# Optimization experiments

Hardware: AMD Instinct MI355X
Metric: run time of the kernel (lower is better)

## Reference

```python
import math
import jax, jax.numpy as jnp
import numpy as np

B, S, D, H = 2, 2048, 768, 12
DK = D // H  # 64
SCALE = math.sqrt(DK)


def setup_inputs() -> dict:
    key = jax.random.key(0)
    ks = jax.random.split(key, 8)
    q = jax.random.normal(ks[0], (B, S, D), dtype=jnp.float32)
    k = jax.random.normal(ks[1], (B, S, D), dtype=jnp.float32)
    v = jax.random.normal(ks[2], (B, S, D), dtype=jnp.float32)
    # causal mask (1 = attend, 0 = masked), per docstring [B, S, S]
    mask = jnp.broadcast_to(jnp.tril(jnp.ones((S, S), dtype=jnp.int32)), (B, S, S))
    std = 1.0 / math.sqrt(D)
    Wq = jax.random.uniform(ks[3], (D, D), jnp.float32, -std, std)
    Wk = jax.random.uniform(ks[4], (D, D), jnp.float32, -std, std)
    Wv = jax.random.uniform(ks[5], (D, D), jnp.float32, -std, std)
    Wo = jax.random.uniform(ks[6], (D, D), jnp.float32, -std, std)
    bo = jax.random.uniform(ks[7], (D,), jnp.float32, -std, std)
    return {"query": q, "key": k, "value": v, "mask": mask,
            "Wq": Wq, "Wk": Wk, "Wv": Wv, "Wo": Wo, "bo": bo}


def reference(query, key, value, mask, Wq, Wk, Wv, Wo, bo):
    # torch Linear: y = x @ W.T (no bias for q/k/v)
    Q = (query @ Wq.T).reshape(B, S, H, DK)  # [B,S,H,dk]
    K = (key @ Wk.T).reshape(B, S, H, DK)
    V = (value @ Wv.T).reshape(B, S, H, DK)
    # scores [B,H,S,S]
    scores = jnp.einsum('bqhd,bkhd->bhqk', Q, K) / SCALE
    scores = jnp.where(mask[:, None, :, :] == 0, jnp.float32(-1e9), scores)
    attention_weights = jax.nn.softmax(scores, axis=-1)
    # dropout is identity in eval mode (reference is deterministic)
    out = jnp.einsum('bhqk,bkhd->bqhd', attention_weights, V).reshape(B, S, D)
    output = out @ Wo.T + bo
    return output, attention_weights
```

## Files before the change

### kernel.cpp

```cpp
#include <hip/hip_runtime.h>
#include <cmath>

constexpr int B = 2, S = 2048, D = 768, H = 12, DK = 64;
constexpr int QKV_N = B * H * S * DK;
constexpr float INV_SCALE = 0.125f;


using bf16x8 = __attribute__((ext_vector_type(8))) short;
using bf16x4 = __attribute__((ext_vector_type(4))) short;
using f32x4  = __attribute__((ext_vector_type(4))) float;

#define DEVI __device__ __forceinline__

DEVI unsigned short f2hi(float x) { union { float f; unsigned u; } c; c.f = x; return (unsigned short)(c.u >> 16); }
DEVI float hi2f(unsigned short h) { union { unsigned u; float f; } c; c.u = (unsigned)h << 16; return c.f; }

DEVI void split8(const float* a, bf16x8& h8, bf16x8& l8) {
  #pragma unroll
  for (int i = 0; i < 8; i++) {
    unsigned short h = f2hi(a[i]);
    h8[i] = (short)h;
    l8[i] = (short)f2hi(a[i] - hi2f(h));
  }
}

DEVI f32x4 mfma3_32(bf16x8 ah, bf16x8 al, bf16x8 bh, bf16x8 bl, f32x4 acc) {
  acc = __builtin_amdgcn_mfma_f32_16x16x32_bf16(al, bh, acc, 0, 0, 0);
  acc = __builtin_amdgcn_mfma_f32_16x16x32_bf16(ah, bl, acc, 0, 0, 0);
  acc = __builtin_amdgcn_mfma_f32_16x16x32_bf16(ah, bh, acc, 0, 0, 0);
  return acc;
}

#if __has_builtin(__builtin_amdgcn_mfma_f32_16x16x16bf16_1k)
DEVI f32x4 mfma16(bf16x4 a, bf16x4 b, f32x4 c) { return __builtin_amdgcn_mfma_f32_16x16x16bf16_1k(a, b, c, 0, 0, 0); }
#elif __has_builtin(__builtin_amdgcn_mfma_f32_16x16x16_bf16_1k)
DEVI f32x4 mfma16(bf16x4 a, bf16x4 b, f32x4 c) { return __builtin_amdgcn_mfma_f32_16x16x16_bf16_1k(a, b, c, 0, 0, 0); }
#elif __has_builtin(__builtin_amdgcn_mfma_f32_16x16x16_bf16)
DEVI f32x4 mfma16(bf16x4 a, bf16x4 b, f32x4 c) { return __builtin_amdgcn_mfma_f32_16x16x16_bf16(a, b, c, 0, 0, 0); }
#else
DEVI f32x4 mfma16(bf16x4 a, bf16x4 b, f32x4 c) {
  asm volatile("v_mfma_f32_16x16x16_bf16 %0, %1, %2, %0" : "+v"(c) : "v"(a), "v"(b));
  return c;
}
#endif

constexpr int PAD = 40;

__global__ __launch_bounds__(512)
void k_qkv_mfma(const float* __restrict__ Xq, const float* __restrict__ Xk,
                const float* __restrict__ Xv,
                const float* __restrict__ Wq, const float* __restrict__ Wk,
                const float* __restrict__ Wv,
                short* __restrict__ Qh, short* __restrict__ Ql,
                short* __restrict__ Kh, short* __restrict__ Kl,
                short* __restrict__ Vh, short* __restrict__ Vl) {
  __shared__ __align__(16) short Ah[128][PAD], Al[128][PAD];
  __shared__ __align__(16) short Bh[128][PAD], Bl[128][PAD];
  const int z = blockIdx.z;
  const float* __restrict__ X = (z == 0) ? Xq : (z == 1) ? Xk : Xv;
  const float* __restrict__ W = (z == 0) ? Wq : (z == 1) ? Wk : Wv;
  short* __restrict__ O_h = (z == 0) ? Qh : (z == 1) ? Kh : Vh;
  short* __restrict__ O_l = (z == 0) ? Ql : (z == 1) ? Kl : Vl;
  const float sc = (z == 0) ? INV_SCALE : 1.0f;
  const int m0 = blockIdx.y * 128, n0 = blockIdx.x * 128;
  const int t = threadIdx.x, wave = t >> 6, lane = t & 63;
  const int wm = (wave >> 1) * 32, wn = (wave & 1) * 64;
  const int srow = t >> 2, sch = (t & 3) * 8;
  const int fr = lane & 15, fk = (lane >> 4) * 8;

  f32x4 acc[2][4];
  #pragma unroll
  for (int i = 0; i < 2; i++)
    #pragma unroll
    for (int j = 0; j < 4; j++) acc[i][j] = (f32x4){0.f, 0.f, 0.f, 0.f};

  for (int k0 = 0; k0 < D; k0 += 32) {
    float abuf[8], bbuf[8];
    *(float4*)&abuf[0] = *(const float4*)&X[(size_t)(m0 + srow) * D + k0 + sch];
    *(float4*)&abuf[4] = *(const float4*)&X[(size_t)(m0 + srow) * D + k0 + sch + 4];
    *(float4*)&bbuf[0] = *(const float4*)&W[(size_t)(n0 + srow) * D + k0 + sch];
    *(float4*)&bbuf[4] = *(const float4*)&W[(size_t)(n0 + srow) * D + k0 + sch + 4];
    bf16x8 h8, l8;
    split8(abuf, h8, l8);
    *(bf16x8*)&Ah[srow][sch] = h8; *(bf16x8*)&Al[srow][sch] = l8;
    split8(bbuf, h8, l8);
    *(bf16x8*)&Bh[srow][sch] = h8; *(bf16x8*)&Bl[srow][sch] = l8;
    __syncthreads();
    bf16x8 a_h[2], a_l[2];
    #pragma unroll
    for (int st = 0; st < 2; st++) {
      a_h[st] = *(const bf16x8*)&Ah[wm + st * 16 + fr][fk];
      a_l[st] = *(const bf16x8*)&Al[wm + st * 16 + fr][fk];
    }
    #pragma unroll
    for (int ct = 0; ct < 4; ct++) {
      bf16x8 b_h = *(const bf16x8*)&Bh[wn + ct * 16 + fr][fk];
      bf16x8 b_l = *(const bf16x8*)&Bl[wn + ct * 16 + fr][fk];
      acc[0][ct] = mfma3_32(a_h[0], a_l[0], b_h, b_l, acc[0][ct]);
      acc[1][ct] = mfma3_32(a_h[1], a_l[1], b_h, b_l, acc[1][ct]);
    }
    __syncthreads();
  }
  #pragma unroll
  for (int st = 0; st < 2; st++)
    #pragma unroll
    for (int ct = 0; ct < 4; ct++)
      #pragma unroll
      for (int r = 0; r < 4; r++) {
        int m = m0 + wm + st * 16 + (lane >> 4) * 4 + r;
        int n = n0 + wn + ct * 16 + (lane & 15);
        int bb = m >> 11, ss = m & (S - 1), hx = n >> 6, dd = n & 63;
        size_t idx = (((size_t)bb * H + hx) * S + ss) * DK + dd;
        float x = acc[st][ct][r] * sc;
        unsigned short xh = f2hi(x);
        O_h[idx] = (short)xh;
        O_l[idx] = (short)f2hi(x - hi2f(xh));
      }
}

constexpr int PADK = 80;
constexpr int PADV = 136;
constexpr int PADC = 132;
constexpr int K_BYTES = 128 * PADK * 2;
constexpr int V_BYTES = 64 * PADV * 2;
constexpr int SMEM_BYTES = 2 * K_BYTES + 2 * V_BYTES;

__global__ __launch_bounds__(512)
void k_attn_fused(const short* __restrict__ Qsh, const short* __restrict__ Qsl,
                  const short* __restrict__ Ksg, const short* __restrict__ Klg,
                  const short* __restrict__ Vsg, const short* __restrict__ Vlg,
                  float* __restrict__ attn, float* __restrict__ ctx) {
  __shared__ __align__(16) char smem[SMEM_BYTES];
  short* Ksh = (short*)smem;
  short* Ksl = (short*)(smem + K_BYTES);
  short* VTh = (short*)(smem + 2 * K_BYTES);
  short* VTl = (short*)(smem + 2 * K_BYTES + V_BYTES);
  float* ctxT = (float*)smem;

  const int qt = 15 - (int)blockIdx.x;
  const int bh = blockIdx.y;
  const int q0 = qt * 128;
  const int kend = (qt + 1) * 128;
  const int t = threadIdx.x, wave = t >> 6, lane = t & 63;
  const int g = lane >> 4, c = lane & 15;
  const int wq = wave * 16;
  const int q = q0 + wq + c;
  const size_t hrow = (size_t)bh * S;

  {
    const int ncols = S - kend;
    if (ncols > 0) {
      const float4 z4 = {0.f, 0.f, 0.f, 0.f};
      for (int rr = 0; rr < 128; ++rr) {
        float* rowp = &attn[(hrow + q0 + rr) * S + kend];
        for (int cc = t * 4; cc < ncols; cc += 2048)
          *(float4*)&rowp[cc] = z4;
      }
    }
  }

  bf16x8 qh0, ql0, qh1, ql1;
  {
    const size_t qb = (hrow + q) * DK + g * 8;
    qh0 = *(const bf16x8*)&Qsh[qb];
    ql0 = *(const bf16x8*)&Qsl[qb];
    qh1 = *(const bf16x8*)&Qsh[qb + 32];
    ql1 = *(const bf16x8*)&Qsl[qb + 32];
  }

  const int srow = t >> 2, sch = (t & 3) * 16;

  float m_run = -3.0e38f, l_run = 0.f;
  for (int kt = 0; kt <= qt; ++kt) {
    {
      const size_t gk = (hrow + (size_t)(kt * 128 + srow)) * DK + sch;
      *(bf16x8*)&Ksh[srow * PADK + sch]     = *(const bf16x8*)&Ksg[gk];
      *(bf16x8*)&Ksh[srow * PADK + sch + 8] = *(const bf16x8*)&Ksg[gk + 8];
      *(bf16x8*)&Ksl[srow * PADK + sch]     = *(const bf16x8*)&Klg[gk];
      *(bf16x8*)&Ksl[srow * PADK + sch + 8] = *(const bf16x8*)&Klg[gk + 8];
    }
    __syncthreads();
    #pragma unroll
    for (int f = 0; f < 8; ++f) {
      const int krow = f * 16 + c;
      bf16x8 kh0 = *(const bf16x8*)&Ksh[krow * PADK + g * 8];
      bf16x8 kl0 = *(const bf16x8*)&Ksl[krow * PADK + g * 8];
      bf16x8 kh1 = *(const bf16x8*)&Ksh[krow * PADK + 32 + g * 8];
      bf16x8 kl1 = *(const bf16x8*)&Ksl[krow * PADK + 32 + g * 8];
      f32x4 s = {0.f, 0.f, 0.f, 0.f};
      s = mfma3_32(kh0, kl0, qh0, ql0, s);
      s = mfma3_32(kh1, kl1, qh1, ql1, s);
      const int kb = kt * 128 + f * 16 + g * 4;
      float tm = -3.0e38f;
      #pragma unroll
      for (int r = 0; r < 4; ++r) {
        float sv = (kb + r <= q) ? s[r] : -3.0e38f;
        tm = fmaxf(tm, sv);
      }
      if (tm > m_run) { l_run *= __expf(m_run - tm); m_run = tm; }
      #pragma unroll
      for (int r = 0; r < 4; ++r)
        l_run += (kb + r <= q) ? __expf(s[r] - m_run) : 0.f;
    }
    __syncthreads();
  }
  #pragma unroll
  for (int off = 16; off <= 32; off <<= 1) {
    float mo = __shfl_xor(m_run, off);
    float lo2 = __shfl_xor(l_run, off);
    float mn = fmaxf(m_run, mo);
    l_run = l_run * __expf(m_run - mn) + lo2 * __expf(mo - mn);
    m_run = mn;
  }
  const float inv_l = 1.0f / l_run;

  f32x4 cacc[4];
  #pragma unroll
  for (int dt = 0; dt < 4; ++dt) cacc[dt] = (f32x4){0.f, 0.f, 0.f, 0.f};

  for (int kt = 0; kt <= qt; ++kt) {
    {
      const size_t gk = (hrow + (size_t)(kt * 128 + srow)) * DK + sch;
      *(bf16x8*)&Ksh[srow * PADK + sch]     = *(const bf16x8*)&Ksg[gk];
      *(bf16x8*)&Ksh[srow * PADK + sch + 8] = *(const bf16x8*)&Ksg[gk + 8];
      *(bf16x8*)&Ksl[srow * PADK + sch]     = *(const bf16x8*)&Klg[gk];
      *(bf16x8*)&Ksl[srow * PADK + sch + 8] = *(const bf16x8*)&Klg[gk + 8];
      bf16x8 vh0 = *(const bf16x8*)&Vsg[gk];
      bf16x8 vh1 = *(const bf16x8*)&Vsg[gk + 8];
      bf16x8 vl0 = *(const bf16x8*)&Vlg[gk];
      bf16x8 vl1 = *(const bf16x8*)&Vlg[gk + 8];
      #pragma unroll
      for (int i = 0; i < 8; ++i) {
        VTh[(sch + i) * PADV + srow]     = vh0[i];
        VTh[(sch + 8 + i) * PADV + srow] = vh1[i];
        VTl[(sch + i) * PADV + srow]     = vl0[i];
        VTl[(sch + 8 + i) * PADV + srow] = vl1[i];
      }
    }
    __syncthreads();
    #pragma unroll
    for (int f = 0; f < 8; ++f) {
      const int krow = f * 16 + c;
      bf16x8 kh0 = *(const bf16x8*)&Ksh[krow * PADK + g * 8];
      bf16x8 kl0 = *(const bf16x8*)&Ksl[krow * PADK + g * 8];
      bf16x8 kh1 = *(const bf16x8*)&Ksh[krow * PADK + 32 + g * 8];
      bf16x8 kl1 = *(const bf16x8*)&Ksl[krow * PADK + 32 + g * 8];
      f32x4 s = {0.f, 0.f, 0.f, 0.f};
      s = mfma3_32(kh0, kl0, qh0, ql0, s);
      s = mfma3_32(kh1, kl1, qh1, ql1, s);
      const int kb = kt * 128 + f * 16 + g * 4;
      float p[4];
      #pragma unroll
      for (int r = 0; r < 4; ++r) {
        float e = __expf(s[r] - m_run) * inv_l;
        p[r] = (kb + r <= q) ? e : 0.f;
      }
      float4 pw = {p[0], p[1], p[2], p[3]};
      *(float4*)&attn[(hrow + q) * S + kb] = pw;
      bf16x4 ph, pl;
      #pragma unroll
      for (int r = 0; r < 4; ++r) {
        unsigned short xh = f2hi(p[r]);
        ph[r] = (short)xh;
        pl[r] = (short)f2hi(p[r] - hi2f(xh));
      }
      #pragma unroll
      for (int dt = 0; dt < 4; ++dt) {
        const int vr = dt * 16 + c;
        bf16x4 vh4 = *(const bf16x4*)&VTh[vr * PADV + f * 16 + g * 4];
        bf16x4 vl4 = *(const bf16x4*)&VTl[vr * PADV + f * 16 + g * 4];
        cacc[dt] = mfma16(vl4, ph, cacc[dt]);
        cacc[dt] = mfma16(vh4, pl, cacc[dt]);
        cacc[dt] = mfma16(vh4, ph, cacc[dt]);
      }
    }
    __syncthreads();
  }

  #pragma unroll
  for (int dt = 0; dt < 4; ++dt)
    #pragma unroll
    for (int r = 0; r < 4; ++r)
      ctxT[(dt * 16 + g * 4 + r) * PADC + wq + c] = cacc[dt][r];
  __syncthreads();
  {
    const int row = t >> 2, ch2 = (t & 3) * 16;
    float buf[16];
    #pragma unroll
    for (int i = 0; i < 16; ++i) buf[i] = ctxT[(ch2 + i) * PADC + row];
    float* cp = &ctx[(hrow + q0 + row) * DK + ch2];
    #pragma unroll
    for (int j = 0; j < 4; ++j)
      *(float4*)&cp[j * 4] = *(const float4*)&buf[j * 4];
  }
}

__global__ __launch_bounds__(512)
void k_oproj_mfma(const float* __restrict__ ctx, const float* __restrict__ Wo,
                  const float* __restrict__ bo, float* __restrict__ out) {
  __shared__ __align__(16) short Ah[128][PAD], Al[128][PAD];
  __shared__ __align__(16) short Bh[128][PAD], Bl[128][PAD];
  const int m0 = blockIdx.y * 128, n0 = blockIdx.x * 128;
  const int t = threadIdx.x, wave = t >> 6, lane = t & 63;
  const int wm = (wave >> 1) * 32, wn = (wave & 1) * 64;
  const int srow = t >> 2, sch = (t & 3) * 8;
  const int fr = lane & 15, fk = (lane >> 4) * 8;

  f32x4 acc[2][4];
  #pragma unroll
  for (int i = 0; i < 2; i++)
    #pragma unroll
    for (int j = 0; j < 4; j++) acc[i][j] = (f32x4){0.f, 0.f, 0.f, 0.f};

  const int am = m0 + srow;
  const int abb = am >> 11, ass = am & (S - 1);
  for (int k0 = 0; k0 < D; k0 += 32) {
    float abuf[8], bbuf[8];
    int kk2 = k0 + sch, hx = kk2 >> 6, dd = kk2 & 63;
    const float* pa = &ctx[(((size_t)abb * H + hx) * S + ass) * DK + dd];
    *(float4*)&abuf[0] = *(const float4*)&pa[0];
    *(float4*)&abuf[4] = *(const float4*)&pa[4];
    *(float4*)&bbuf[0] = *(const float4*)&Wo[(size_t)(n0 + srow) * D + k0 + sch];
    *(float4*)&bbuf[4] = *(const float4*)&Wo[(size_t)(n0 + srow) * D + k0 + sch + 4];
    bf16x8 h8, l8;
    split8(abuf, h8, l8);
    *(bf16x8*)&Ah[srow][sch] = h8; *(bf16x8*)&Al[srow][sch] = l8;
    split8(bbuf, h8, l8);
    *(bf16x8*)&Bh[srow][sch] = h8; *(bf16x8*)&Bl[srow][sch] = l8;
    __syncthreads();
    bf16x8 a_h[2], a_l[2];
    #pragma unroll
    for (int st = 0; st < 2; st++) {
      a_h[st] = *(const bf16x8*)&Ah[wm + st * 16 + fr][fk];
      a_l[st] = *(const bf16x8*)&Al[wm + st * 16 + fr][fk];
    }
    #pragma unroll
    for (int ct = 0; ct < 4; ct++) {
      bf16x8 b_h = *(const bf16x8*)&Bh[wn + ct * 16 + fr][fk];
      bf16x8 b_l = *(const bf16x8*)&Bl[wn + ct * 16 + fr][fk];
      acc[0][ct] = mfma3_32(a_h[0], a_l[0], b_h, b_l, acc[0][ct]);
      acc[1][ct] = mfma3_32(a_h[1], a_l[1], b_h, b_l, acc[1][ct]);
    }
    __syncthreads();
  }
  #pragma unroll
  for (int st = 0; st < 2; st++)
    #pragma unroll
    for (int ct = 0; ct < 4; ct++)
      #pragma unroll
      for (int r = 0; r < 4; r++) {
        int m = m0 + wm + st * 16 + (lane >> 4) * 4 + r;
        int n = n0 + wn + ct * 16 + (lane & 15);
        out[(size_t)m * D + n] = acc[st][ct][r] + bo[n];
      }
}

extern "C" void kernel_launch(void* const* d_in, const int* in_sizes, int n_in,
                              void* d_out, int out_size, void* d_ws, size_t ws_size,
                              hipStream_t stream) {
  (void)in_sizes; (void)n_in; (void)out_size; (void)ws_size;
  const float* q  = (const float*)d_in[0];
  const float* k  = (const float*)d_in[1];
  const float* v  = (const float*)d_in[2];
  const float* Wq = (const float*)d_in[4];
  const float* Wk = (const float*)d_in[5];
  const float* Wv = (const float*)d_in[6];
  const float* Wo = (const float*)d_in[7];
  const float* bo = (const float*)d_in[8];

  float* out  = (float*)d_out;
  float* attn = out + (size_t)B * S * D;

  short* Qh = (short*)d_ws;
  short* Ql = Qh + (size_t)QKV_N;
  short* Kh = Ql + (size_t)QKV_N;
  short* Kl = Kh + (size_t)QKV_N;
  short* Vh = Kl + (size_t)QKV_N;
  short* Vl = Vh + (size_t)QKV_N;
  float* ctx = (float*)(Vl + (size_t)QKV_N);

  k_qkv_mfma<<<dim3(6, 32, 3), 512, 0, stream>>>(q, k, v, Wq, Wk, Wv,
                                                 Qh, Ql, Kh, Kl, Vh, Vl);
  k_attn_fused<<<dim3(16, 24), 512, 0, stream>>>(Qh, Ql, Kh, Kl, Vh, Vl, attn, ctx);
  k_oproj_mfma<<<dim3(6, 32), 512, 0, stream>>>(ctx, Wo, bo, out);
}
```

Before: 743.2 us.

## Shrink attention tiles to 64 rows, prefetch K/V into registers, swizzle V transpose

The fused attention kernel now uses 64-query tiles with 256-thread blocks (32x24 grid), which doubles block count and should improve occupancy and causal load balance. K/V tiles for the next iteration are loaded into registers during compute on the current tile, hiding global latency behind the MFMA work. The transposed V store/read uses an XOR swizzle with smaller padding to cut LDS bank conflicts and shared memory footprint. Smaller tiles add more barriers per key and reload K/V more often across blocks, and register prefetch raises register pressure.

```diff
diff --git a/kernel.cpp b/kernel.cpp
--- a/kernel.cpp
+++ b/kernel.cpp
@@ -118,42 +118,41 @@
       }
 }
 
-constexpr int PADK = 80;
-constexpr int PADV = 136;
-constexpr int PADC = 132;
-constexpr int K_BYTES = 128 * PADK * 2;
-constexpr int V_BYTES = 64 * PADV * 2;
-constexpr int SMEM_BYTES = 2 * K_BYTES + 2 * V_BYTES;
-
-__global__ __launch_bounds__(512)
+constexpr int PADK2 = 68;
+constexpr int PADV2 = 68;
+constexpr int PADC2 = 65;
+constexpr int KB2   = 64 * PADK2;
+constexpr int VB2   = 64 * PADV2;
+constexpr int SMEM2 = (2 * KB2 + 2 * VB2) * 2;
+
+__global__ __launch_bounds__(256, 4)
 void k_attn_fused(const short* __restrict__ Qsh, const short* __restrict__ Qsl,
                   const short* __restrict__ Ksg, const short* __restrict__ Klg,
                   const short* __restrict__ Vsg, const short* __restrict__ Vlg,
                   float* __restrict__ attn, float* __restrict__ ctx) {
-  __shared__ __align__(16) char smem[SMEM_BYTES];
+  __shared__ __align__(16) char smem[SMEM2];
   short* Ksh = (short*)smem;
-  short* Ksl = (short*)(smem + K_BYTES);
-  short* VTh = (short*)(smem + 2 * K_BYTES);
-  short* VTl = (short*)(smem + 2 * K_BYTES + V_BYTES);
+  short* Ksl = Ksh + KB2;
+  short* VTh = Ksl + KB2;
+  short* VTl = VTh + VB2;
   float* ctxT = (float*)smem;
 
-  const int qt = 15 - (int)blockIdx.x;
+  const int jt = 31 - (int)blockIdx.x;
   const int bh = blockIdx.y;
-  const int q0 = qt * 128;
-  const int kend = (qt + 1) * 128;
+  const int q0 = jt * 64;
   const int t = threadIdx.x, wave = t >> 6, lane = t & 63;
   const int g = lane >> 4, c = lane & 15;
-  const int wq = wave * 16;
-  const int q = q0 + wq + c;
+  const int q = q0 + wave * 16 + c;
   const size_t hrow = (size_t)bh * S;
 
   {
-    const int ncols = S - kend;
+    const int zc0 = q0 + 64;
+    const int ncols = S - zc0;
     if (ncols > 0) {
       const float4 z4 = {0.f, 0.f, 0.f, 0.f};
-      for (int rr = 0; rr < 128; ++rr) {
-        float* rowp = &attn[(hrow + q0 + rr) * S + kend];
-        for (int cc = t * 4; cc < ncols; cc += 2048)
+      for (int rr = 0; rr < 64; ++rr) {
+        float* rowp = &attn[(hrow + q0 + rr) * S + zc0];
+        for (int cc = t * 4; cc < ncols; cc += 1024)
           *(float4*)&rowp[cc] = z4;
       }
     }
@@ -162,47 +161,57 @@
   bf16x8 qh0, ql0, qh1, ql1;
   {
     const size_t qb = (hrow + q) * DK + g * 8;
-    qh0 = *(const bf16x8*)&Qsh[qb];
-    ql0 = *(const bf16x8*)&Qsl[qb];
-    qh1 = *(const bf16x8*)&Qsh[qb + 32];
-    ql1 = *(const bf16x8*)&Qsl[qb + 32];
-  }
-
-  const int srow = t >> 2, sch = (t & 3) * 16;
+    qh0 = *(const bf16x8*)&Qsh[qb];      ql0 = *(const bf16x8*)&Qsl[qb];
+    qh1 = *(const bf16x8*)&Qsh[qb + 32]; ql1 = *(const bf16x8*)&Qsl[qb + 32];
+  }
+
+  const int srow = t >> 2;
+  const int sch = (t & 3) * 16;
+  const int vcol = srow ^ ((t & 3) * 8);
 
   float m_run = -3.0e38f, l_run = 0.f;
-  for (int kt = 0; kt <= qt; ++kt) {
+  {
+    bf16x8 kr[4];
     {
-      const size_t gk = (hrow + (size_t)(kt * 128 + srow)) * DK + sch;
-      *(bf16x8*)&Ksh[srow * PADK + sch]     = *(const bf16x8*)&Ksg[gk];
-      *(bf16x8*)&Ksh[srow * PADK + sch + 8] = *(const bf16x8*)&Ksg[gk + 8];
-      *(bf16x8*)&Ksl[srow * PADK + sch]     = *(const bf16x8*)&Klg[gk];
-      *(bf16x8*)&Ksl[srow * PADK + sch + 8] = *(const bf16x8*)&Klg[gk + 8];
-    }
-    __syncthreads();
-    #pragma unroll
-    for (int f = 0; f < 8; ++f) {
-      const int krow = f * 16 + c;
-      bf16x8 kh0 = *(const bf16x8*)&Ksh[krow * PADK + g * 8];
-      bf16x8 kl0 = *(const bf16x8*)&Ksl[krow * PADK + g * 8];
-      bf16x8 kh1 = *(const bf16x8*)&Ksh[krow * PADK + 32 + g * 8];
-      bf16x8 kl1 = *(const bf16x8*)&Ksl[krow * PADK + 32 + g * 8];
-      f32x4 s = {0.f, 0.f, 0.f, 0.f};
-      s = mfma3_32(kh0, kl0, qh0, ql0, s);
-      s = mfma3_32(kh1, kl1, qh1, ql1, s);
-      const int kb = kt * 128 + f * 16 + g * 4;
-      float tm = -3.0e38f;
+      const size_t gk = (hrow + (size_t)srow) * DK + sch;
+      kr[0] = *(const bf16x8*)&Ksg[gk]; kr[1] = *(const bf16x8*)&Ksg[gk + 8];
+      kr[2] = *(const bf16x8*)&Klg[gk]; kr[3] = *(const bf16x8*)&Klg[gk + 8];
+    }
+    for (int kt = 0; kt <= jt; ++kt) {
+      __syncthreads();
+      *(bf16x8*)&Ksh[srow * PADK2 + sch]     = kr[0];
+      *(bf16x8*)&Ksh[srow * PADK2 + sch + 8] = kr[1];
+      *(bf16x8*)&Ksl[srow * PADK2 + sch]     = kr[2];
+      *(bf16x8*)&Ksl[srow * PADK2 + sch + 8] = kr[3];
+      __syncthreads();
+      if (kt < jt) {
+        const size_t gk = (hrow + (size_t)((kt + 1) * 64 + srow)) * DK + sch;
+        kr[0] = *(const bf16x8*)&Ksg[gk]; kr[1] = *(const bf16x8*)&Ksg[gk + 8];
+        kr[2] = *(const bf16x8*)&Klg[gk]; kr[3] = *(const bf16x8*)&Klg[gk + 8];
+      }
       #pragma unroll
-      for (int r = 0; r < 4; ++r) {
-        float sv = (kb + r <= q) ? s[r] : -3.0e38f;
-        tm = fmaxf(tm, sv);
-      }
-      if (tm > m_run) { l_run *= __expf(m_run - tm); m_run = tm; }
-      #pragma unroll
-      for (int r = 0; r < 4; ++r)
-        l_run += (kb + r <= q) ? __expf(s[r] - m_run) : 0.f;
-    }
-    __syncthreads();
+      for (int f = 0; f < 4; ++f) {
+        const int krow = f * 16 + c;
+        bf16x8 kh0 = *(const bf16x8*)&Ksh[krow * PADK2 + g * 8];
+        bf16x8 kl0 = *(const bf16x8*)&Ksl[krow * PADK2 + g * 8];
+        bf16x8 kh1 = *(const bf16x8*)&Ksh[krow * PADK2 + 32 + g * 8];
+        bf16x8 kl1 = *(const bf16x8*)&Ksl[krow * PADK2 + 32 + g * 8];
+        f32x4 s = {0.f, 0.f, 0.f, 0.f};
+        s = mfma3_32(kh0, kl0, qh0, ql0, s);
+        s = mfma3_32(kh1, kl1, qh1, ql1, s);
+        const int kb = kt * 64 + f * 16 + g * 4;
+        float tm = -3.0e38f;
+        #pragma unroll
+        for (int r = 0; r < 4; ++r) {
+          float sv = (kb + r <= q) ? s[r] : -3.0e38f;
+          tm = fmaxf(tm, sv);
+        }
+        if (tm > m_run) { l_run *= __expf(m_run - tm); m_run = tm; }
+        #pragma unroll
+        for (int r = 0; r < 4; ++r)
+          l_run += (kb + r <= q) ? __expf(s[r] - m_run) : 0.f;
+      }
+    }
   }
   #pragma unroll
   for (int off = 16; off <= 32; off <<= 1) {
@@ -218,82 +227,95 @@
   #pragma unroll
   for (int dt = 0; dt < 4; ++dt) cacc[dt] = (f32x4){0.f, 0.f, 0.f, 0.f};
 
-  for (int kt = 0; kt <= qt; ++kt) {
+  {
+    bf16x8 kvr[8];
     {
-      const size_t gk = (hrow + (size_t)(kt * 128 + srow)) * DK + sch;
-      *(bf16x8*)&Ksh[srow * PADK + sch]     = *(const bf16x8*)&Ksg[gk];
-      *(bf16x8*)&Ksh[srow * PADK + sch + 8] = *(const bf16x8*)&Ksg[gk + 8];
-      *(bf16x8*)&Ksl[srow * PADK + sch]     = *(const bf16x8*)&Klg[gk];
-      *(bf16x8*)&Ksl[srow * PADK + sch + 8] = *(const bf16x8*)&Klg[gk + 8];
-      bf16x8 vh0 = *(const bf16x8*)&Vsg[gk];
-      bf16x8 vh1 = *(const bf16x8*)&Vsg[gk + 8];
-      bf16x8 vl0 = *(const bf16x8*)&Vlg[gk];
-      bf16x8 vl1 = *(const bf16x8*)&Vlg[gk + 8];
+      const size_t gk = (hrow + (size_t)srow) * DK + sch;
+      kvr[0] = *(const bf16x8*)&Ksg[gk]; kvr[1] = *(const bf16x8*)&Ksg[gk + 8];
+      kvr[2] = *(const bf16x8*)&Klg[gk]; kvr[3] = *(const bf16x8*)&Klg[gk + 8];
+      kvr[4] = *(const bf16x8*)&Vsg[gk]; kvr[5] = *(const bf16x8*)&Vsg[gk + 8];
+      kvr[6] = *(const bf16x8*)&Vlg[gk]; kvr[7] = *(const bf16x8*)&Vlg[gk + 8];
+    }
+    for (int kt = 0; kt <= jt; ++kt) {
+      __syncthreads();
+      *(bf16x8*)&Ksh[srow * PADK2 + sch]     = kvr[0];
+      *(bf16x8*)&Ksh[srow * PADK2 + sch + 8] = kvr[1];
+      *(bf16x8*)&Ksl[srow * PADK2 + sch]     = kvr[2];
+      *(bf16x8*)&Ksl[srow * PADK2 + sch + 8] = kvr[3];
       #pragma unroll
       for (int i = 0; i < 8; ++i) {
-        VTh[(sch + i) * PADV + srow]     = vh0[i];
-        VTh[(sch + 8 + i) * PADV + srow] = vh1[i];
-        VTl[(sch + i) * PADV + srow]     = vl0[i];
-        VTl[(sch + 8 + i) * PADV + srow] = vl1[i];
-      }
-    }
-    __syncthreads();
-    #pragma unroll
-    for (int f = 0; f < 8; ++f) {
-      const int krow = f * 16 + c;
-      bf16x8 kh0 = *(const bf16x8*)&Ksh[krow * PADK + g * 8];
-      bf16x8 kl0 = *(const bf16x8*)&Ksl[krow * PADK + g * 8];
-      bf16x8 kh1 = *(const bf16x8*)&Ksh[krow * PADK + 32 + g * 8];
-      bf16x8 kl1 = *(const bf16x8*)&Ksl[krow * PADK + 32 + g * 8];
-      f32x4 s = {0.f, 0.f, 0.f, 0.f};
-      s = mfma3_32(kh0, kl0, qh0, ql0, s);
-      s = mfma3_32(kh1, kl1, qh1, ql1, s);
-      const int kb = kt * 128 + f * 16 + g * 4;
-      float p[4];
+        VTh[(sch + i) * PADV2 + vcol]     = kvr[4][i];
+        VTh[(sch + 8 + i) * PADV2 + vcol] = kvr[5][i];
+        VTl[(sch + i) * PADV2 + vcol]     = kvr[6][i];
+        VTl[(sch + 8 + i) * PADV2 + vcol] = kvr[7][i];
+      }
+      __syncthreads();
+      if (kt < jt) {
+        const size_t gk = (hrow + (size_t)((kt + 1) * 64 + srow)) * DK + sch;
+        kvr[0] = *(const bf16x8*)&Ksg[gk]; kvr[1] = *(const bf16x8*)&Ksg[gk + 8];
+        kvr[2] = *(const bf16x8*)&Klg[gk]; kvr[3] = *(const bf16x8*)&Klg[gk + 8];
+        kvr[4] = *(const bf16x8*)&Vsg[gk]; kvr[5] = *(const bf16x8*)&Vsg[gk + 8];
+        kvr[6] = *(const bf16x8*)&Vlg[gk]; kvr[7] = *(const bf16x8*)&Vlg[gk + 8];
+      }
       #pragma unroll
-      for (int r = 0; r < 4; ++r) {
-        float e = __expf(s[r] - m_run) * inv_l;
-        p[r] = (kb + r <= q) ? e : 0.f;
-      }
-      float4 pw = {p[0], p[1], p[2], p[3]};
-      *(float4*)&attn[(hrow + q) * S + kb] = pw;
-      bf16x4 ph, pl;
-      #pragma unroll
-      for (int r = 0; r < 4; ++r) {
-        unsigned short xh = f2hi(p[r]);
-        ph[r] = (short)xh;
-        pl[r] = (short)f2hi(p[r] - hi2f(xh));
-      }
-      #pragma unroll
-      for (int dt = 0; dt < 4; ++dt) {
-        const int vr = dt * 16 + c;
-        bf16x4 vh4 = *(const bf16x4*)&VTh[vr * PADV + f * 16 + g * 4];
-        bf16x4 vl4 = *(const bf16x4*)&VTl[vr * PADV + f * 16 + g * 4];
-        cacc[dt] = mfma16(vl4, ph, cacc[dt]);
-        cacc[dt] = mfma16(vh4, pl, cacc[dt]);
-        cacc[dt] = mfma16(vh4, ph, cacc[dt]);
-      }
-    }
-    __syncthreads();
-  }
-
+      for (int f = 0; f < 4; ++f) {
+        const int krow = f * 16 + c;
+        bf16x8 kh0 = *(const bf16x8*)&Ksh[krow * PADK2 + g * 8];
+        bf16x8 kl0 = *(const bf16x8*)&Ksl[krow * PADK2 + g * 8];
+        bf16x8 kh1 = *(const bf16x8*)&Ksh[krow * PADK2 + 32 + g * 8];
+        bf16x8 kl1 = *(const bf16x8*)&Ksl[krow * PADK2 + 32 + g * 8];
+        f32x4 s = {0.f, 0.f, 0.f, 0.f};
+        s = mfma3_32(kh0, kl0, qh0, ql0, s);
+        s = mfma3_32(kh1, kl1, qh1, ql1, s);
+        const int kb = kt * 64 + f * 16 + g * 4;
+        float p[4];
+        #pragma unroll
+        for (int r = 0; r < 4; ++r) {
+          float e = __expf(s[r] - m_run) * inv_l;
+          p[r] = (kb + r <= q) ? e : 0.f;
+        }
+        float4 pw = {p[0], p[1], p[2], p[3]};
+        *(float4*)&attn[(hrow + q) * S + kb] = pw;
+        bf16x4 ph, pl;
+        #pragma unroll
+        for (int r = 0; r < 4; ++r) {
+          unsigned short xh = f2hi(p[r]);
+          ph[r] = (short)xh;
+          pl[r] = (short)f2hi(p[r] - hi2f(xh));
+        }
+        const int kc = (f * 16 + g * 4);
+        #pragma unroll
+        for (int dt = 0; dt < 4; ++dt) {
+          const int kcs = kc ^ (dt * 8);
+          bf16x4 vh4 = *(const bf16x4*)&VTh[(dt * 16 + c) * PADV2 + kcs];
+          bf16x4 vl4 = *(const bf16x4*)&VTl[(dt * 16 + c) * PADV2 + kcs];
+          cacc[dt] = mfma16(vl4, ph, cacc[dt]);
+          cacc[dt] = mfma16(vh4, pl, cacc[dt]);
+          cacc[dt] = mfma16(vh4, ph, cacc[dt]);
+        }
+      }
+    }
+  }
+
+  __syncthreads();
   #pragma unroll
   for (int dt = 0; dt < 4; ++dt)
     #pragma unroll
     for (int r = 0; r < 4; ++r)
-      ctxT[(dt * 16 + g * 4 + r) * PADC + wq + c] = cacc[dt][r];
+      ctxT[(dt * 16 + g * 4 + r) * PADC2 + wave * 16 + c] = cacc[dt][r];
   __syncthreads();
   {
-    const int row = t >> 2, ch2 = (t & 3) * 16;
+    const int qrow = t >> 2, ch2 = (t & 3) * 16;
     float buf[16];
     #pragma unroll
-    for (int i = 0; i < 16; ++i) buf[i] = ctxT[(ch2 + i) * PADC + row];
-    float* cp = &ctx[(hrow + q0 + row) * DK + ch2];
+    for (int i = 0; i < 16; ++i) buf[i] = ctxT[(ch2 + i) * PADC2 + qrow];
+    float* cp = &ctx[(hrow + q0 + qrow) * DK + ch2];
     #pragma unroll
     for (int j = 0; j < 4; ++j)
       *(float4*)&cp[j * 4] = *(const float4*)&buf[j * 4];
   }
 }
+
 
 __global__ __launch_bounds__(512)
 void k_oproj_mfma(const float* __restrict__ ctx, const float* __restrict__ Wo,
@@ -381,6 +403,6 @@
 
   k_qkv_mfma<<<dim3(6, 32, 3), 512, 0, stream>>>(q, k, v, Wq, Wk, Wv,
                                                  Qh, Ql, Kh, Kl, Vh, Vl);
-  k_attn_fused<<<dim3(16, 24), 512, 0, stream>>>(Qh, Ql, Kh, Kl, Vh, Vl, attn, ctx);
+  k_attn_fused<<<dim3(32, 24), 256, 0, stream>>>(Qh, Ql, Kh, Kl, Vh, Vl, attn, ctx);
   k_oproj_mfma<<<dim3(6, 32), 512, 0, stream>>>(ctx, Wo, bo, out);
 }
```

New measurement: 975.5 us. 31.2% more time.
